# Optimization experiments

Hardware: AMD Instinct MI355X
Metric: run time of the kernel (lower is better)

## Reference

```python
import jax, jax.numpy as jnp
import numpy as np

N_ATOM = 4096
NHEADS = 8
C_PER_HEAD = 64
BLOCK_SIZE = 128
LOCAL_WINDOW = 512


def setup_inputs() -> dict:
    key = jax.random.key(0)
    k1, k2, k3, k4 = jax.random.split(key, 4)
    q = jax.random.normal(k1, (N_ATOM, NHEADS, C_PER_HEAD), dtype=jnp.float32)
    k = jax.random.normal(k2, (N_ATOM, NHEADS, C_PER_HEAD), dtype=jnp.float32)
    v = jax.random.normal(k3, (N_ATOM, NHEADS, C_PER_HEAD), dtype=jnp.float32)
    pair_bias = jax.random.normal(k4, (N_ATOM, N_ATOM, NHEADS), dtype=jnp.float32)
    return {"q": q, "k": k, "v": v, "pair_bias": pair_bias}


def reference(q, k, v, pair_bias):
    # Local block-sparse attention: banded blockmask with blocks_per_side
    # = max(1, local_window // block_size) blocks on each side of the diagonal.
    # NOTE: pair_bias is accepted by the original forward but never used
    # (it is not passed to block_sparse_attn_func), so it is ignored here.
    N, H, D = q.shape
    B = BLOCK_SIZE
    bps = max(1, LOCAL_WINDOW // BLOCK_SIZE)  # blocks per side = 4
    nrow = N // B  # N is a multiple of block_size here
    scale = jnp.asarray(D, q.dtype) ** -0.5  # softmax_scale=None -> 1/sqrt(d)

    qb = q.reshape(nrow, B, H, D)
    kb = k.reshape(nrow, B, H, D)
    vb = v.reshape(nrow, B, H, D)

    offs = jnp.arange(-bps, bps + 1)                      # [W], W = 2*bps+1
    cols = jnp.arange(nrow)[:, None] + offs[None, :]      # [nrow, W]
    valid = (cols >= 0) & (cols < nrow)                   # band edge mask
    colsc = jnp.clip(cols, 0, nrow - 1)

    kg = kb[colsc]  # [nrow, W, B, H, D] -- only band blocks gathered
    vg = vb[colsc]

    # scores: [nrow, H, B, W, B]
    scores = jnp.einsum('rihd,rwjhd->rhiwj', qb, kg) * scale
    neg_inf = jnp.asarray(-jnp.inf, scores.dtype)
    scores = jnp.where(valid[:, None, None, :, None], scores, neg_inf)

    p = jax.nn.softmax(scores.reshape(nrow, H, B, -1), axis=-1)
    p = p.reshape(scores.shape)

    out = jnp.einsum('rhiwj,rwjhd->rihd', p, vg)  # [nrow, B, H, D]
    return out.reshape(N, H, D)
```

## Files before the change

kernel.cpp:

```cpp
#include <hip/hip_runtime.h>
#include <hip/hip_bf16.h>

#define NATOM 4096
#define NH 8
#define DIMD 64
#define BLK 128
#define NROW 32
#define BPS 4
#define ROWSTRIDE (NH * DIMD)
#define SCALE 0.125f
#define L2E 1.4426950408889634f

#define K_LD 72
#define V_LD 136
#define P_LD 136

#define HEAD_ELEMS (NATOM * DIMD)
#define WS_NEEDED  (2u * NH * HEAD_ELEMS * 2u)

typedef __attribute__((ext_vector_type(8))) short bf16x8;
typedef __attribute__((ext_vector_type(4))) float f32x4;
typedef __attribute__((ext_vector_type(4))) unsigned int u32x4;

__device__ __forceinline__ short f2bf(float x) {
    unsigned int u = __builtin_bit_cast(unsigned int, x);
    unsigned int r = (u + 0x7fffu + ((u >> 16) & 1u)) >> 16;
    return (short)r;
}
__device__ __forceinline__ unsigned int cvtpk(float lo, float hi) {
    unsigned int r;
    asm("v_cvt_pk_bf16_f32 %0, %1, %2" : "=v"(r) : "v"(lo), "v"(hi));
    return r;
}
__device__ __forceinline__ f32x4 vmax4(f32x4 a, f32x4 b) {
    f32x4 r;
    r[0] = fmaxf(a[0], b[0]); r[1] = fmaxf(a[1], b[1]);
    r[2] = fmaxf(a[2], b[2]); r[3] = fmaxf(a[3], b[3]);
    return r;
}

extern "C" __global__ __launch_bounds__(256)
void prep_kernel(const float* __restrict__ k, const float* __restrict__ v,
                 short* __restrict__ Kb, short* __restrict__ Vt)
{
    __shared__ short Tr[DIMD * V_LD];
    const int bid  = blockIdx.x;
    const int h    = bid & 7;
    const int part = bid >> 3;
    const int t    = threadIdx.x;

    if (part < 32) {
        const int nb = part;
        #pragma unroll
        for (int i = 0; i < 4; ++i) {
            int idx = i * 256 + t;
            int row = idx >> 3;
            int d0  = (idx & 7) * 8;
            const float* src = k + (size_t)(nb * BLK + row) * ROWSTRIDE + h * DIMD + d0;
            float4 a = *(const float4*)src;
            float4 c = *(const float4*)(src + 4);
            bf16x8 f;
            f[0] = f2bf(a.x); f[1] = f2bf(a.y); f[2] = f2bf(a.z); f[3] = f2bf(a.w);
            f[4] = f2bf(c.x); f[5] = f2bf(c.y); f[6] = f2bf(c.z); f[7] = f2bf(c.w);
            *(bf16x8*)(Kb + (size_t)h * HEAD_ELEMS + (size_t)(nb * BLK + row) * DIMD + d0) = f;
        }
    } else {
        const int nb = part - 32;
        const int vd = t & 63;
        const int g  = t >> 6;
        const float* vp = v + (size_t)(nb * BLK) * ROWSTRIDE + h * DIMD + vd;
        #pragma unroll
        for (int i = 0; i < 8; ++i) {
            int n4 = i * 16 + g * 4;
            const float* vr = vp + (size_t)n4 * ROWSTRIDE;
            short4 s4;
            s4.x = f2bf(vr[0 * ROWSTRIDE]);
            s4.y = f2bf(vr[1 * ROWSTRIDE]);
            s4.z = f2bf(vr[2 * ROWSTRIDE]);
            s4.w = f2bf(vr[3 * ROWSTRIDE]);
            *(short4*)&Tr[vd * V_LD + n4] = s4;
        }
        __syncthreads();
        #pragma unroll
        for (int i = 0; i < 4; ++i) {
            int s  = i * 256 + t;
            int d  = s >> 4;
            int c8 = (s & 15) * 8;
            int kc = c8 >> 5;
            int l2 = (c8 >> 3) & 3;
            int kA = kc * 32 + l2 * 4;
            short4 a  = *(const short4*)&Tr[d * V_LD + kA];
            short4 c4 = *(const short4*)&Tr[d * V_LD + kA + 16];
            bf16x8 f;
            f[0] = a.x;  f[1] = a.y;  f[2] = a.z;  f[3] = a.w;
            f[4] = c4.x; f[5] = c4.y; f[6] = c4.z; f[7] = c4.w;
            *(bf16x8*)(Vt + (size_t)h * HEAD_ELEMS + (size_t)d * NATOM + nb * BLK + c8) = f;
        }
    }
}

extern "C" __global__ __launch_bounds__(256)
void bsattn_main(const float* __restrict__ q,
                 const short* __restrict__ Kb,
                 const short* __restrict__ Vt,
                 float* __restrict__ out)
{
    __shared__ short Ksh[2][BLK * K_LD];
    __shared__ short Vsh[2][DIMD * V_LD];

    const int bid = blockIdx.x;
    const int h   = bid & 7;
    const int br  = bid >> 3;
    const int r   = br >> 1;
    const int t   = threadIdx.x;
    const int w   = t >> 6;
    const int lane = t & 63;
    const int lr = lane >> 4;
    const int lc = lane & 15;

    const int qbase = br * 64 + w * 16;
    const float* qp = q + (size_t)(qbase + lc) * ROWSTRIDE + h * DIMD + lr * 8;
    bf16x8 qf[2];
    #pragma unroll
    for (int kc = 0; kc < 2; ++kc) {
        float4 a = *(const float4*)(qp + kc * 32);
        float4 b = *(const float4*)(qp + kc * 32 + 4);
        bf16x8 f;
        f[0] = f2bf(a.x * SCALE); f[1] = f2bf(a.y * SCALE);
        f[2] = f2bf(a.z * SCALE); f[3] = f2bf(a.w * SCALE);
        f[4] = f2bf(b.x * SCALE); f[5] = f2bf(b.y * SCALE);
        f[6] = f2bf(b.z * SCALE); f[7] = f2bf(b.w * SCALE);
        qf[kc] = f;
    }

    const short* kbase = Kb + (size_t)h * HEAD_ELEMS;
    const short* vbase = Vt + (size_t)h * HEAD_ELEMS;

    f32x4 acc[4] = {};
    float m_run = -1e30f, l_run = 0.0f;

    const int kb0 = (r - BPS > 0) ? (r - BPS) : 0;
    const int kb1 = (r + BPS < NROW - 1) ? (r + BPS) : (NROW - 1);

    const short* kg = kbase + (size_t)kb0 * BLK * DIMD;
    const short* vg = vbase + (size_t)kb0 * BLK;
    bf16x8 kpre[4], vpre[4];

#define LOADREGS()                                                              \
    {                                                                           \
        _Pragma("unroll")                                                       \
        for (int i = 0; i < 4; ++i) {                                           \
            int s = i * 256 + t;                                                \
            kpre[i] = *(const bf16x8*)(kg + (size_t)(s >> 3) * DIMD + (s & 7) * 8); \
            vpre[i] = *(const bf16x8*)(vg + (size_t)(s >> 4) * NATOM + (s & 15) * 8); \
        }                                                                       \
        kg += BLK * DIMD; vg += BLK;                                            \
    }

#define STAGE(buf)                                                              \
    {                                                                           \
        _Pragma("unroll")                                                       \
        for (int i = 0; i < 4; ++i) {                                           \
            int s = i * 256 + t;                                                \
            *(bf16x8*)&Ksh[buf][(s >> 3) * K_LD + (s & 7) * 8] = kpre[i];       \
            *(bf16x8*)&Vsh[buf][(s >> 4) * V_LD + (s & 15) * 8] = vpre[i];      \
        }                                                                       \
    }

    LOADREGS();
    STAGE(0);
    if (kb0 < kb1) LOADREGS();
    __syncthreads();

    int cur = 0;
    for (int kb = kb0; kb <= kb1; ++kb) {
        const short* ks = &Ksh[cur][0];
        const short* vs = &Vsh[cur][0];

        f32x4 s[8];
        __builtin_amdgcn_s_setprio(1);
        #pragma unroll
        for (int mt = 0; mt < 8; ++mt) {
            f32x4 z = {};
            #pragma unroll
            for (int kc = 0; kc < 2; ++kc) {
                bf16x8 kf = *(const bf16x8*)&ks[(mt * 16 + lc) * K_LD + kc * 32 + lr * 8];
                z = __builtin_amdgcn_mfma_f32_16x16x32_bf16(kf, qf[kc], z, 0, 0, 0);
            }
            s[mt] = z;
        }
        __builtin_amdgcn_s_setprio(0);

        f32x4 a0 = vmax4(vmax4(s[0], s[1]), vmax4(s[2], s[3]));
        f32x4 a1 = vmax4(vmax4(s[4], s[5]), vmax4(s[6], s[7]));
        a0 = vmax4(a0, a1);
        float mx = fmaxf(fmaxf(a0[0], a0[1]), fmaxf(a0[2], a0[3]));
        mx = fmaxf(mx, __shfl_xor(mx, 16, 64));
        mx = fmaxf(mx, __shfl_xor(mx, 32, 64));
        if (__any(mx > m_run + 8.0f)) {
            float mnew = fmaxf(m_run, mx);
            float al = __builtin_amdgcn_exp2f((m_run - mnew) * L2E);
            m_run = mnew;
            l_run *= al;
            #pragma unroll
            for (int dn = 0; dn < 4; ++dn) {
                acc[dn][0] *= al; acc[dn][1] *= al;
                acc[dn][2] *= al; acc[dn][3] *= al;
            }
        }
        f32x4 sv = {};
        #pragma unroll
        for (int mt = 0; mt < 8; ++mt) {
            #pragma unroll
            for (int e = 0; e < 4; ++e) {
                float p = __builtin_amdgcn_exp2f((s[mt][e] - m_run) * L2E);
                s[mt][e] = p;
                sv[e] += p;
            }
        }
        float sum = (sv[0] + sv[1]) + (sv[2] + sv[3]);
        sum += __shfl_xor(sum, 16, 64);
        sum += __shfl_xor(sum, 32, 64);
        l_run += sum;

        bf16x8 pf[4];
        #pragma unroll
        for (int kc = 0; kc < 4; ++kc) {
            u32x4 pk;
            pk[0] = cvtpk(s[2 * kc][0],     s[2 * kc][1]);
            pk[1] = cvtpk(s[2 * kc][2],     s[2 * kc][3]);
            pk[2] = cvtpk(s[2 * kc + 1][0], s[2 * kc + 1][1]);
            pk[3] = cvtpk(s[2 * kc + 1][2], s[2 * kc + 1][3]);
            pf[kc] = __builtin_bit_cast(bf16x8, pk);
        }

        __builtin_amdgcn_s_setprio(1);
        #pragma unroll
        for (int dn = 0; dn < 4; ++dn) {
            f32x4 o = acc[dn];
            #pragma unroll
            for (int kc = 0; kc < 4; ++kc) {
                bf16x8 vf = *(const bf16x8*)&vs[(dn * 16 + lc) * V_LD + kc * 32 + lr * 8];
                o = __builtin_amdgcn_mfma_f32_16x16x32_bf16(vf, pf[kc], o, 0, 0, 0);
            }
            acc[dn] = o;
        }
        __builtin_amdgcn_s_setprio(0);

        if (kb < kb1) {
            STAGE(cur ^ 1);
            if (kb + 1 < kb1) LOADREGS();
        }
        __syncthreads();
        cur ^= 1;
    }

    float inv = 1.0f / l_run;
    float* orow = out + (size_t)(qbase + lc) * ROWSTRIDE + h * DIMD;
    #pragma unroll
    for (int dn = 0; dn < 4; ++dn) {
        f32x4 rv;
        rv[0] = acc[dn][0] * inv; rv[1] = acc[dn][1] * inv;
        rv[2] = acc[dn][2] * inv; rv[3] = acc[dn][3] * inv;
        *(float4*)(orow + dn * 16 + lr * 4) = *(float4*)&rv;
    }
#undef LOADREGS
#undef STAGE
}

extern "C" __global__ __launch_bounds__(512)
void bsattn_fallback(const float* __restrict__ q,
                     const float* __restrict__ k,
                     const float* __restrict__ v,
                     float* __restrict__ out)
{
    __shared__ short Ksh[BLK * K_LD];
    __shared__ short Vsh[DIMD * V_LD];
    __shared__ short Psh[8][16 * P_LD];

    const int r = blockIdx.x;
    const int h = blockIdx.y;
    const int t = threadIdx.x;
    const int w = t >> 6;
    const int lane = t & 63;
    const int lr = lane >> 4;
    const int lc = lane & 15;

    const int krow = t >> 4;
    const int kcol = (t & 15) * 4;
    const int vd  = t & 63;
    const int vkg = t >> 6;

    const int qrow_l = w * 16 + lc;
    const float* qp = q + (size_t)(r * BLK + qrow_l) * ROWSTRIDE + h * DIMD + lr * 8;
    bf16x8 qf[2];
    #pragma unroll
    for (int kc = 0; kc < 2; ++kc) {
        float4 a = *(const float4*)(qp + kc * 32);
        float4 b = *(const float4*)(qp + kc * 32 + 4);
        bf16x8 f;
        f[0] = f2bf(a.x); f[1] = f2bf(a.y); f[2] = f2bf(a.z); f[3] = f2bf(a.w);
        f[4] = f2bf(b.x); f[5] = f2bf(b.y); f[6] = f2bf(b.z); f[7] = f2bf(b.w);
        qf[kc] = f;
    }

    f32x4 acc[4] = {};
    float m_run[4], l_run[4];
    #pragma unroll
    for (int i = 0; i < 4; ++i) { m_run[i] = -1e30f; l_run[i] = 0.0f; }

    const int kb0 = (r - BPS > 0) ? (r - BPS) : 0;
    const int kb1 = (r + BPS < NROW - 1) ? (r + BPS) : (NROW - 1);

    for (int kb = kb0; kb <= kb1; ++kb) {
        __syncthreads();
        const float* kp = k + (size_t)(kb * BLK) * ROWSTRIDE + h * DIMD;
        const float* vp = v + (size_t)(kb * BLK) * ROWSTRIDE + h * DIMD;

        #pragma unroll
        for (int i = 0; i < 4; ++i) {
            float4 kv = *(const float4*)(kp + (size_t)(i * 32 + krow) * ROWSTRIDE + kcol);
            short4 ks;
            ks.x = f2bf(kv.x); ks.y = f2bf(kv.y); ks.z = f2bf(kv.z); ks.w = f2bf(kv.w);
            *(short4*)&Ksh[(i * 32 + krow) * K_LD + kcol] = ks;

            const float* vr = vp + (size_t)(i * 32 + vkg * 4) * ROWSTRIDE + vd;
            short4 vs;
            vs.x = f2bf(vr[0 * ROWSTRIDE]);
            vs.y = f2bf(vr[1 * ROWSTRIDE]);
            vs.z = f2bf(vr[2 * ROWSTRIDE]);
            vs.w = f2bf(vr[3 * ROWSTRIDE]);
            *(short4*)&Vsh[vd * V_LD + i * 32 + vkg * 4] = vs;
        }
        __syncthreads();

        f32x4 s[8];
        #pragma unroll
        for (int n = 0; n < 8; ++n) {
            f32x4 z = {};
            #pragma unroll
            for (int kc = 0; kc < 2; ++kc) {
                bf16x8 kf = *(const bf16x8*)&Ksh[(n * 16 + lc) * K_LD + kc * 32 + lr * 8];
                z = __builtin_amdgcn_mfma_f32_16x16x32_bf16(qf[kc], kf, z, 0, 0, 0);
            }
            s[n] = z * SCALE;
        }

        #pragma unroll
        for (int rr = 0; rr < 4; ++rr) {
            float mx = s[0][rr];
            #pragma unroll
            for (int n = 1; n < 8; ++n) mx = fmaxf(mx, s[n][rr]);
            #pragma unroll
            for (int off = 1; off < 16; off <<= 1)
                mx = fmaxf(mx, __shfl_xor(mx, off, 64));
            float mnew = fmaxf(m_run[rr], mx);
            float al = exp2f((m_run[rr] - mnew) * L2E);
            m_run[rr] = mnew;
            float sum = 0.0f;
            #pragma unroll
            for (int n = 0; n < 8; ++n) {
                float p = exp2f((s[n][rr] - mnew) * L2E);
                s[n][rr] = p;
                sum += p;
            }
            #pragma unroll
            for (int off = 1; off < 16; off <<= 1)
                sum += __shfl_xor(sum, off, 64);
            l_run[rr] = l_run[rr] * al + sum;
            #pragma unroll
            for (int dn = 0; dn < 4; ++dn) acc[dn][rr] *= al;
        }

        short* pw = &Psh[w][0];
        #pragma unroll
        for (int n = 0; n < 8; ++n) {
            #pragma unroll
            for (int rr = 0; rr < 4; ++rr) {
                pw[(lr * 4 + rr) * P_LD + n * 16 + lc] = f2bf(s[n][rr]);
            }
        }

        #pragma unroll
        for (int dn = 0; dn < 4; ++dn) {
            f32x4 o = acc[dn];
            #pragma unroll
            for (int kc = 0; kc < 4; ++kc) {
                bf16x8 pf = *(const bf16x8*)&pw[lc * P_LD + kc * 32 + lr * 8];
                bf16x8 vf = *(const bf16x8*)&Vsh[(dn * 16 + lc) * V_LD + kc * 32 + lr * 8];
                o = __builtin_amdgcn_mfma_f32_16x16x32_bf16(pf, vf, o, 0, 0, 0);
            }
            acc[dn] = o;
        }
    }

    float* op = out + (size_t)(r * BLK + w * 16) * ROWSTRIDE + h * DIMD;
    #pragma unroll
    for (int rr = 0; rr < 4; ++rr) {
        float inv = 1.0f / l_run[rr];
        float* orow = op + (size_t)(lr * 4 + rr) * ROWSTRIDE;
        #pragma unroll
        for (int dn = 0; dn < 4; ++dn) {
            orow[dn * 16 + lc] = acc[dn][rr] * inv;
        }
    }
}

extern "C" void kernel_launch(void* const* d_in, const int* in_sizes, int n_in,
                              void* d_out, int out_size, void* d_ws, size_t ws_size,
                              hipStream_t stream) {
    const float* q = (const float*)d_in[0];
    const float* k = (const float*)d_in[1];
    const float* v = (const float*)d_in[2];
    float* out = (float*)d_out;

    if (ws_size >= (size_t)WS_NEEDED) {
        short* Kb = (short*)d_ws;
        short* Vt = Kb + (size_t)NH * HEAD_ELEMS;
        prep_kernel<<<512, 256, 0, stream>>>(k, v, Kb, Vt);
        bsattn_main<<<512, 256, 0, stream>>>(q, Kb, Vt, out);
    } else {
        bsattn_fallback<<<dim3(NROW, NH), 512, 0, stream>>>(q, k, v, out);
    }
}
```

Measured before the change: 33.10 us.

## Fuse K/V bf16 prep and attention into one cooperative kernel with grid sync

Merges the K/V conversion and transpose prep pass with the main block-sparse attention kernel into a single cooperative launch. A grid-wide barrier separates the two phases, and Q fragments are loaded and scaled before the barrier. The goal is to remove one kernel launch and the gap between dependent launches. In exchange it pays for a grid-wide sync, relies on all 512 blocks being co-resident (launch_bounds 256,2), and falls back to the two-kernel path if the cooperative launch fails.

```diff
diff --git a/kernel.cpp b/kernel.cpp
--- a/kernel.cpp
+++ b/kernel.cpp
@@ -1,5 +1,6 @@
 #include <hip/hip_runtime.h>
 #include <hip/hip_bf16.h>
+#include <hip/hip_cooperative_groups.h>
 
 #define NATOM 4096
 #define NH 8
@@ -37,6 +38,232 @@
     r[0] = fmaxf(a[0], b[0]); r[1] = fmaxf(a[1], b[1]);
     r[2] = fmaxf(a[2], b[2]); r[3] = fmaxf(a[3], b[3]);
     return r;
+}
+
+extern "C" __global__ __launch_bounds__(256, 2)
+void bsattn_fused(const float* __restrict__ q,
+                  const float* __restrict__ k,
+                  const float* __restrict__ v,
+                  short* __restrict__ Kb,
+                  short* __restrict__ Vt,
+                  float* __restrict__ out)
+{
+    __shared__ short Ksh[2][BLK * K_LD];
+    __shared__ short Vsh[2][DIMD * V_LD];
+
+    const int bid  = blockIdx.x;
+    const int h    = bid & 7;
+    const int t    = threadIdx.x;
+
+    {
+        const int part = bid >> 3;
+        if (part < 32) {
+            const int nb = part;
+            #pragma unroll
+            for (int i = 0; i < 4; ++i) {
+                int idx = i * 256 + t;
+                int row = idx >> 3;
+                int d0  = (idx & 7) * 8;
+                const float* src = k + (size_t)(nb * BLK + row) * ROWSTRIDE + h * DIMD + d0;
+                float4 a = *(const float4*)src;
+                float4 c = *(const float4*)(src + 4);
+                bf16x8 f;
+                f[0] = f2bf(a.x); f[1] = f2bf(a.y); f[2] = f2bf(a.z); f[3] = f2bf(a.w);
+                f[4] = f2bf(c.x); f[5] = f2bf(c.y); f[6] = f2bf(c.z); f[7] = f2bf(c.w);
+                *(bf16x8*)(Kb + (size_t)h * HEAD_ELEMS + (size_t)(nb * BLK + row) * DIMD + d0) = f;
+            }
+        } else {
+            short* Tr = &Ksh[0][0];
+            const int nb = part - 32;
+            const int vd = t & 63;
+            const int g  = t >> 6;
+            const float* vp = v + (size_t)(nb * BLK) * ROWSTRIDE + h * DIMD + vd;
+            #pragma unroll
+            for (int i = 0; i < 8; ++i) {
+                int n4 = i * 16 + g * 4;
+                const float* vr = vp + (size_t)n4 * ROWSTRIDE;
+                short4 s4;
+                s4.x = f2bf(vr[0 * ROWSTRIDE]);
+                s4.y = f2bf(vr[1 * ROWSTRIDE]);
+                s4.z = f2bf(vr[2 * ROWSTRIDE]);
+                s4.w = f2bf(vr[3 * ROWSTRIDE]);
+                *(short4*)&Tr[vd * V_LD + n4] = s4;
+            }
+            __syncthreads();
+            #pragma unroll
+            for (int i = 0; i < 4; ++i) {
+                int s  = i * 256 + t;
+                int d  = s >> 4;
+                int c8 = (s & 15) * 8;
+                int kc = c8 >> 5;
+                int l2 = (c8 >> 3) & 3;
+                int kA = kc * 32 + l2 * 4;
+                short4 a  = *(const short4*)&Tr[d * V_LD + kA];
+                short4 c4 = *(const short4*)&Tr[d * V_LD + kA + 16];
+                bf16x8 f;
+                f[0] = a.x;  f[1] = a.y;  f[2] = a.z;  f[3] = a.w;
+                f[4] = c4.x; f[5] = c4.y; f[6] = c4.z; f[7] = c4.w;
+                *(bf16x8*)(Vt + (size_t)h * HEAD_ELEMS + (size_t)d * NATOM + nb * BLK + c8) = f;
+            }
+        }
+    }
+
+    const int br  = bid >> 3;
+    const int r   = br >> 1;
+    const int w   = t >> 6;
+    const int lane = t & 63;
+    const int lr = lane >> 4;
+    const int lc = lane & 15;
+
+    const int qbase = br * 64 + w * 16;
+    const float* qp = q + (size_t)(qbase + lc) * ROWSTRIDE + h * DIMD + lr * 8;
+    bf16x8 qf[2];
+    #pragma unroll
+    for (int kc = 0; kc < 2; ++kc) {
+        float4 a = *(const float4*)(qp + kc * 32);
+        float4 b = *(const float4*)(qp + kc * 32 + 4);
+        bf16x8 f;
+        f[0] = f2bf(a.x * (SCALE * L2E)); f[1] = f2bf(a.y * (SCALE * L2E));
+        f[2] = f2bf(a.z * (SCALE * L2E)); f[3] = f2bf(a.w * (SCALE * L2E));
+        f[4] = f2bf(b.x * (SCALE * L2E)); f[5] = f2bf(b.y * (SCALE * L2E));
+        f[6] = f2bf(b.z * (SCALE * L2E)); f[7] = f2bf(b.w * (SCALE * L2E));
+        qf[kc] = f;
+    }
+    bf16x8 onesA;
+    #pragma unroll
+    for (int i = 0; i < 8; ++i) onesA[i] = (short)0x3F80;
+
+    cooperative_groups::this_grid().sync();
+
+    const short* kbase = Kb + (size_t)h * HEAD_ELEMS;
+    const short* vbase = Vt + (size_t)h * HEAD_ELEMS;
+
+    f32x4 acc[4] = {};
+    f32x4 lacc = {};
+    float m_run = -1e30f;
+
+    const int kb0 = (r - BPS > 0) ? (r - BPS) : 0;
+    const int kb1 = (r + BPS < NROW - 1) ? (r + BPS) : (NROW - 1);
+
+    const short* kg = kbase + (size_t)kb0 * BLK * DIMD;
+    const short* vg = vbase + (size_t)kb0 * BLK;
+    bf16x8 kpre[4], vpre[4];
+
+#define LOADREGS()                                                              \
+    {                                                                           \
+        _Pragma("unroll")                                                       \
+        for (int i = 0; i < 4; ++i) {                                           \
+            int s = i * 256 + t;                                                \
+            kpre[i] = *(const bf16x8*)(kg + (size_t)(s >> 3) * DIMD + (s & 7) * 8); \
+            vpre[i] = *(const bf16x8*)(vg + (size_t)(s >> 4) * NATOM + (s & 15) * 8); \
+        }                                                                       \
+        kg += BLK * DIMD; vg += BLK;                                            \
+    }
+
+#define STAGE(buf)                                                              \
+    {                                                                           \
+        _Pragma("unroll")                                                       \
+        for (int i = 0; i < 4; ++i) {                                           \
+            int s = i * 256 + t;                                                \
+            *(bf16x8*)&Ksh[buf][(s >> 3) * K_LD + (s & 7) * 8] = kpre[i];       \
+            *(bf16x8*)&Vsh[buf][(s >> 4) * V_LD + (s & 15) * 8] = vpre[i];      \
+        }                                                                       \
+    }
+
+    LOADREGS();
+    STAGE(0);
+    if (kb0 < kb1) LOADREGS();
+    __syncthreads();
+
+    int cur = 0;
+    for (int kb = kb0; kb <= kb1; ++kb) {
+        const short* ks = &Ksh[cur][0];
+        const short* vs = &Vsh[cur][0];
+
+        f32x4 s[8];
+        __builtin_amdgcn_s_setprio(1);
+        #pragma unroll
+        for (int mt = 0; mt < 8; ++mt) {
+            f32x4 z = {};
+            #pragma unroll
+            for (int kc = 0; kc < 2; ++kc) {
+                bf16x8 kf = *(const bf16x8*)&ks[(mt * 16 + lc) * K_LD + kc * 32 + lr * 8];
+                z = __builtin_amdgcn_mfma_f32_16x16x32_bf16(kf, qf[kc], z, 0, 0, 0);
+            }
+            s[mt] = z;
+        }
+        __builtin_amdgcn_s_setprio(0);
+
+        f32x4 a0 = vmax4(vmax4(s[0], s[1]), vmax4(s[2], s[3]));
+        f32x4 a1 = vmax4(vmax4(s[4], s[5]), vmax4(s[6], s[7]));
+        a0 = vmax4(a0, a1);
+        float mx = fmaxf(fmaxf(a0[0], a0[1]), fmaxf(a0[2], a0[3]));
+        mx = fmaxf(mx, __shfl_xor(mx, 16, 64));
+        mx = fmaxf(mx, __shfl_xor(mx, 32, 64));
+        if (__any(mx > m_run + 8.0f)) {
+            float mnew = fmaxf(m_run, mx);
+            float al = __builtin_amdgcn_exp2f(m_run - mnew);
+            m_run = mnew;
+            #pragma unroll
+            for (int dn = 0; dn < 4; ++dn) {
+                acc[dn][0] *= al; acc[dn][1] *= al;
+                acc[dn][2] *= al; acc[dn][3] *= al;
+            }
+            lacc[0] *= al; lacc[1] *= al; lacc[2] *= al; lacc[3] *= al;
+        }
+        #pragma unroll
+        for (int mt = 0; mt < 8; ++mt) {
+            #pragma unroll
+            for (int e = 0; e < 4; ++e)
+                s[mt][e] = __builtin_amdgcn_exp2f(s[mt][e] - m_run);
+        }
+
+        bf16x8 pf[4];
+        #pragma unroll
+        for (int kc = 0; kc < 4; ++kc) {
+            u32x4 pk;
+            pk[0] = cvtpk(s[2 * kc][0],     s[2 * kc][1]);
+            pk[1] = cvtpk(s[2 * kc][2],     s[2 * kc][3]);
+            pk[2] = cvtpk(s[2 * kc + 1][0], s[2 * kc + 1][1]);
+            pk[3] = cvtpk(s[2 * kc + 1][2], s[2 * kc + 1][3]);
+            pf[kc] = __builtin_bit_cast(bf16x8, pk);
+        }
+
+        __builtin_amdgcn_s_setprio(1);
+        #pragma unroll
+        for (int dn = 0; dn < 4; ++dn) {
+            f32x4 o = acc[dn];
+            #pragma unroll
+            for (int kc = 0; kc < 4; ++kc) {
+                bf16x8 vf = *(const bf16x8*)&vs[(dn * 16 + lc) * V_LD + kc * 32 + lr * 8];
+                o = __builtin_amdgcn_mfma_f32_16x16x32_bf16(vf, pf[kc], o, 0, 0, 0);
+            }
+            acc[dn] = o;
+        }
+        #pragma unroll
+        for (int kc = 0; kc < 4; ++kc)
+            lacc = __builtin_amdgcn_mfma_f32_16x16x32_bf16(onesA, pf[kc], lacc, 0, 0, 0);
+        __builtin_amdgcn_s_setprio(0);
+
+        if (kb < kb1) {
+            STAGE(cur ^ 1);
+            if (kb + 1 < kb1) LOADREGS();
+        }
+        __syncthreads();
+        cur ^= 1;
+    }
+
+    float inv = 1.0f / lacc[0];
+    float* orow = out + (size_t)(qbase + lc) * ROWSTRIDE + h * DIMD;
+    #pragma unroll
+    for (int dn = 0; dn < 4; ++dn) {
+        f32x4 rv;
+        rv[0] = acc[dn][0] * inv; rv[1] = acc[dn][1] * inv;
+        rv[2] = acc[dn][2] * inv; rv[3] = acc[dn][3] * inv;
+        *(float4*)(orow + dn * 16 + lr * 4) = *(float4*)&rv;
+    }
+#undef LOADREGS
+#undef STAGE
 }
 
 extern "C" __global__ __launch_bounds__(256)
@@ -417,8 +644,14 @@
     if (ws_size >= (size_t)WS_NEEDED) {
         short* Kb = (short*)d_ws;
         short* Vt = Kb + (size_t)NH * HEAD_ELEMS;
-        prep_kernel<<<512, 256, 0, stream>>>(k, v, Kb, Vt);
-        bsattn_main<<<512, 256, 0, stream>>>(q, Kb, Vt, out);
+        void* args[] = {(void*)&q, (void*)&k, (void*)&v,
+                        (void*)&Kb, (void*)&Vt, (void*)&out};
+        hipError_t err = hipLaunchCooperativeKernel(
+            (const void*)bsattn_fused, dim3(512), dim3(256), args, 0, stream);
+        if (err != hipSuccess) {
+            prep_kernel<<<512, 256, 0, stream>>>(k, v, Kb, Vt);
+            bsattn_main<<<512, 256, 0, stream>>>(q, Kb, Vt, out);
+        }
     } else {
         bsattn_fallback<<<dim3(NROW, NH), 512, 0, stream>>>(q, k, v, out);
     }
```

Result: slower. 104.1 us (+214.6%).
